# Kernel tuning notes

Measured on AMD Instinct MI355X. Metric: run time of the kernel, lower is better.

Reference implementation:

```python
import jax, jax.numpy as jnp
import numpy as np

B, R, L, K = 64, 196, 512, 768
NEG = jnp.float32(-2**31 + 1)


def setup_inputs() -> dict:
    key = jax.random.key(0)
    ks = jax.random.split(key, 8)
    image_emb = jax.random.normal(ks[0], (B, R, L), dtype=jnp.float32)
    seq_emb = jax.random.normal(ks[1], (B, L, K), dtype=jnp.float32)
    mask = jax.random.randint(ks[2], (B, L), 0, 2, dtype=jnp.int32)
    # Linear(l,1) and Linear(k,1) params, Xavier-ish scale
    image_W = jax.random.normal(ks[3], (L, 1), dtype=jnp.float32) / np.sqrt(L)
    image_b = jnp.zeros((1,), dtype=jnp.float32)
    seq_W = jax.random.normal(ks[4], (K, 1), dtype=jnp.float32) / np.sqrt(K)
    seq_b = jnp.zeros((1,), dtype=jnp.float32)
    # V_weight [L, L], xavier_uniform
    lim = np.sqrt(6.0 / (L + L)).astype(np.float32)
    V_weight = jax.random.uniform(ks[5], (L, L), dtype=jnp.float32, minval=-lim, maxval=lim)
    return {"image_emb": image_emb, "seq_emb": seq_emb, "mask": mask,
            "image_W": image_W, "image_b": image_b,
            "seq_W": seq_W, "seq_b": seq_b, "V_weight": V_weight}


def reference(image_emb, seq_emb, mask, image_W, image_b, seq_W, seq_b, V_weight):
    # p: [B,R,1], q: [B,L,1]
    p = jnp.tanh(image_emb @ image_W + image_b)
    q = jnp.tanh(seq_emb @ seq_W + seq_b)
    qt = jnp.swapaxes(q, 1, 2)              # [B,1,L]
    emb = p @ qt + qt                       # [B,R,L] (rank-1 outer + broadcast add)
    score = emb @ V_weight                  # [B,R,L]
    # dropout_rate=0.0 -> identity
    score = jnp.where(mask[:, None, :] == 0, NEG, score)
    score = jax.nn.softmax(score, axis=-1)  # [B,R,L]
    out = score @ seq_emb                   # [B,R,K]
    out = out / jnp.sqrt(jnp.float32(seq_emb.shape[-1]))
    return out
```

## Files before the change

kernel.cpp:

```cpp
#include <hip/hip_runtime.h>
#include <cstdint>
#include <cstddef>


typedef __attribute__((ext_vector_type(8))) short short8;
typedef __attribute__((ext_vector_type(4))) float f32x4;

__device__ __forceinline__ unsigned short f32_to_bf16(float x) {
    unsigned int u = __float_as_uint(x);
    unsigned int r = (u + 0x7FFFu + ((u >> 16) & 1u)) >> 16;
    return (unsigned short)r;
}
__device__ __forceinline__ float bf16_to_f32(unsigned short h) {
    return __uint_as_float(((unsigned int)h) << 16);
}

__global__ __launch_bounds__(256) void krows_p(const float* __restrict__ x,
                                               const float* __restrict__ w,
                                               const float* __restrict__ bias,
                                               float* __restrict__ outp) {
    int wv = threadIdx.x >> 6, lane = threadIdx.x & 63;
    int row = blockIdx.x * 4 + wv;
    const float4* x4 = (const float4*)(x + (size_t)row * 512);
    const float4* w4 = (const float4*)w;
    float s = 0.f;
#pragma unroll
    for (int i = 0; i < 2; ++i) {
        float4 a = x4[i * 64 + lane];
        float4 c = w4[i * 64 + lane];
        s += a.x * c.x + a.y * c.y + a.z * c.z + a.w * c.w;
    }
#pragma unroll
    for (int o = 32; o; o >>= 1) s += __shfl_xor(s, o, 64);
    if (lane == 0) outp[row] = tanhf(s + bias[0]);
}

__global__ __launch_bounds__(256) void krows_q(const float* __restrict__ x,
                                               const float* __restrict__ w,
                                               const float* __restrict__ bias,
                                               float* __restrict__ outp) {
    int wv = threadIdx.x >> 6, lane = threadIdx.x & 63;
    int row = blockIdx.x * 4 + wv;
    const float4* x4 = (const float4*)(x + (size_t)row * 768);
    const float4* w4 = (const float4*)w;
    float s = 0.f;
#pragma unroll
    for (int i = 0; i < 3; ++i) {
        float4 a = x4[i * 64 + lane];
        float4 c = w4[i * 64 + lane];
        s += a.x * c.x + a.y * c.y + a.z * c.z + a.w * c.w;
    }
#pragma unroll
    for (int o = 32; o; o >>= 1) s += __shfl_xor(s, o, 64);
    if (lane == 0) outp[row] = tanhf(s + bias[0]);
}

__global__ __launch_bounds__(256) void kw(const float* __restrict__ qv,
                                          const float* __restrict__ V,
                                          const int* __restrict__ mask,
                                          float* __restrict__ wm) {
    __shared__ __align__(16) float sq[512];
    __shared__ __align__(16) float sacc[8][32][4];
    int b = blockIdx.x >> 2, jc = blockIdx.x & 3;
    int t = threadIdx.x;
    sq[t] = qv[b * 512 + t];
    sq[t + 256] = qv[b * 512 + t + 256];
    __syncthreads();
    int jt = t & 31, lg = t >> 5;
    const float4* V4 = (const float4*)V;
    int col4 = jc * 32 + jt;
    float ax = 0.f, ay = 0.f, az = 0.f, aw = 0.f;
    int lbase = lg * 64;
#pragma unroll 8
    for (int li = 0; li < 64; ++li) {
        int l = lbase + li;
        float qq = sq[l];
        float4 v = V4[(size_t)l * 128 + col4];
        ax += qq * v.x; ay += qq * v.y; az += qq * v.z; aw += qq * v.w;
    }
    sacc[lg][jt][0] = ax; sacc[lg][jt][1] = ay;
    sacc[lg][jt][2] = az; sacc[lg][jt][3] = aw;
    __syncthreads();
    if (t < 32) {
        float sx = 0.f, sy = 0.f, sz = 0.f, sw = 0.f;
#pragma unroll
        for (int g = 0; g < 8; ++g) {
            sx += sacc[g][t][0]; sy += sacc[g][t][1];
            sz += sacc[g][t][2]; sw += sacc[g][t][3];
        }
        const int* mrow = mask + b * 512 + jc * 128 + t * 4;
        float4 o;
        o.x = mrow[0] ? sx : -1e30f;
        o.y = mrow[1] ? sy : -1e30f;
        o.z = mrow[2] ? sz : -1e30f;
        o.w = mrow[3] ? sw : -1e30f;
        ((float4*)(wm + b * 512 + jc * 128))[t] = o;
    }
}

__global__ __launch_bounds__(256, 2) void kattn(const float* __restrict__ seq,
                                                const float* __restrict__ p,
                                                const float* __restrict__ wm,
                                                float* __restrict__ out) {
    __shared__ __align__(16) unsigned int sseq[2][128 * 32];
    __shared__ __align__(16) float swm[512];
    __shared__ float sinvz[64];
    __shared__ float sred[16];

    int id = blockIdx.x;
    int rt = id & 3;
    int nt = (id >> 2) % 6;
    int b  = id / 24;
    int t  = threadIdx.x;
    int wv = t >> 6, lane = t & 63;
    int mm = lane & 15, q = lane >> 4;
    int nb = nt * 128;

    float v0 = wm[b * 512 + t];
    float v1 = wm[b * 512 + t + 256];
    swm[t] = v0; swm[t + 256] = v1;
    float lmax = fmaxf(v0, v1);
    float fa = (v0 > -1e29f) ? v0 : 1e30f;
    float fb = (v1 > -1e29f) ? v1 : 1e30f;
    float lmin = fminf(fa, fb);
#pragma unroll
    for (int o = 32; o; o >>= 1) {
        lmax = fmaxf(lmax, __shfl_xor(lmax, o, 64));
        lmin = fminf(lmin, __shfl_xor(lmin, o, 64));
    }
    if (lane == 0) { sred[wv] = lmax; sred[8 + wv] = lmin; }
    __syncthreads();
    float wmax = fmaxf(fmaxf(sred[0], sred[1]), fmaxf(sred[2], sred[3]));
    float wmin = fminf(fminf(sred[8], sred[9]), fminf(sred[10], sred[11]));

    int rl = wv * 16 + mm;
    int r  = rt * 64 + rl;
    bool valid = r < 196;
    int pidx = b * 196 + (valid ? r : 195);
    float c = 1.0f + p[pidx];
    float M = (c >= 0.f) ? c * wmax : c * wmin;

    short8 afrag[16];
    float zsum = 0.f;
    const f32x4* swm4 = (const f32x4*)swm;
#pragma unroll
    for (int tk = 0; tk < 16; ++tk) {
        int jb = tk * 32 + q * 8;
        f32x4 w0 = swm4[jb >> 2];
        f32x4 w1 = swm4[(jb >> 2) + 1];
        short8 af;
#pragma unroll
        for (int jj = 0; jj < 8; ++jj) {
            float ww = (jj < 4) ? w0[jj] : w1[jj - 4];
            float e = valid ? __expf(c * ww - M) : 0.f;
            unsigned short h = f32_to_bf16(e);
            zsum += bf16_to_f32(h);
            af[jj] = (short)h;
        }
        afrag[tk] = af;
    }
    zsum += __shfl_xor(zsum, 16, 64);
    zsum += __shfl_xor(zsum, 32, 64);
    if (q == 0) sinvz[rl] = 1.0f / zsum;

    f32x4 acc[8];
#pragma unroll
    for (int s = 0; s < 8; ++s) acc[s] = (f32x4){0.f, 0.f, 0.f, 0.f};

    const float* seqb = seq + (size_t)b * 512 * 768 + nb;
    int tl = t & 31, jp = t >> 5;
    int n0 = tl * 4;
    auto stage = [&](int ch, int buf) {
        unsigned int* sb = sseq[buf];
#pragma unroll
        for (int pass = 0; pass < 4; ++pass) {
            int jl = pass * 16 + jp * 2;
            int jglob = ch * 64 + jl;
            float4 a0 = *(const float4*)(seqb + (size_t)jglob * 768 + n0);
            float4 a1 = *(const float4*)(seqb + (size_t)(jglob + 1) * 768 + n0);
            float a0v[4] = {a0.x, a0.y, a0.z, a0.w};
            float a1v[4] = {a1.x, a1.y, a1.z, a1.w};
            int g = jl >> 3;
            int wo = (jl & 7) >> 1;
#pragma unroll
            for (int i = 0; i < 4; ++i) {
                int n = n0 + i;
                int sw = (n ^ (n >> 3)) & 7;
                unsigned int pk = (unsigned int)f32_to_bf16(a0v[i]) |
                                  ((unsigned int)f32_to_bf16(a1v[i]) << 16);
                sb[n * 32 + ((g ^ sw) << 2) + wo] = pk;
            }
        }
    };

    __syncthreads();
    stage(0, 0);
    __syncthreads();
#pragma unroll
    for (int ch = 0; ch < 8; ++ch) {
        if (ch < 7) stage(ch + 1, (ch + 1) & 1);
        const unsigned int* cb = sseq[ch & 1];
#pragma unroll
        for (int kk = 0; kk < 2; ++kk) {
            short8 bfr[8];
#pragma unroll
            for (int s = 0; s < 8; ++s) {
                int n = s * 16 + mm;
                int g = kk * 4 + q;
                int sw = (n ^ (n >> 3)) & 7;
                bfr[s] = *(const short8*)(cb + n * 32 + ((g ^ sw) << 2));
            }
#pragma unroll
            for (int s = 0; s < 8; ++s)
                acc[s] = __builtin_amdgcn_mfma_f32_16x16x32_bf16(
                    afrag[ch * 2 + kk], bfr[s], acc[s], 0, 0, 0);
        }
        __syncthreads();
    }

    const float invsqrtk = 0.036084391824351615f;
#pragma unroll
    for (int reg = 0; reg < 4; ++reg) {
        int row = q * 4 + reg;
        int rr = rt * 64 + wv * 16 + row;
        if (rr < 196) {
            float scale = sinvz[wv * 16 + row] * invsqrtk;
            float* op = out + (size_t)(b * 196 + rr) * 768 + nb + mm;
#pragma unroll
            for (int s = 0; s < 8; ++s)
                op[s * 16] = acc[s][reg] * scale;
        }
    }
}

extern "C" void kernel_launch(void* const* d_in, const int* in_sizes, int n_in,
                              void* d_out, int out_size, void* d_ws, size_t ws_size,
                              hipStream_t stream) {
    const float* image_emb = (const float*)d_in[0];
    const float* seq_emb   = (const float*)d_in[1];
    const int*   mask      = (const int*)d_in[2];
    const float* image_W   = (const float*)d_in[3];
    const float* image_b   = (const float*)d_in[4];
    const float* seq_W     = (const float*)d_in[5];
    const float* seq_b     = (const float*)d_in[6];
    const float* V         = (const float*)d_in[7];
    float* out = (float*)d_out;

    float* p_ws  = (float*)d_ws;
    float* q_ws  = (float*)((char*)d_ws + (64 << 10));
    float* wm_ws = (float*)((char*)d_ws + (192 << 10));

    krows_p<<<dim3(3136), dim3(256), 0, stream>>>(image_emb, image_W, image_b, p_ws);
    krows_q<<<dim3(8192), dim3(256), 0, stream>>>(seq_emb, seq_W, seq_b, q_ws);
    kw<<<dim3(256), dim3(256), 0, stream>>>(q_ws, V, mask, wm_ws);
    kattn<<<dim3(1536), dim3(256), 0, stream>>>(seq_emb, p_ws, wm_ws, out);
}
```

Measured before the change: 257.6 us.

## Fuse q projection with bf16 transpose of seq_emb and use transposed MFMA attention

Adds a kernel that reads seq_emb once, computes the q projection, and writes a bf16 transposed copy (K-major) to workspace. A new attention kernel stages tiles of that copy into swizzled LDS with double buffering and feeds bf16 MFMA directly, with a block-index remap for locality. The intent is to halve the bytes the attention kernel reads and make its B-operand loads contiguous, in exchange for writing a 50MB intermediate. The old path remains as a fallback when the workspace is too small.

```diff
diff --git a/kernel.cpp b/kernel.cpp
--- a/kernel.cpp
+++ b/kernel.cpp
@@ -53,6 +53,60 @@
 #pragma unroll
     for (int o = 32; o; o >>= 1) s += __shfl_xor(s, o, 64);
     if (lane == 0) outp[row] = tanhf(s + bias[0]);
+}
+
+__global__ __launch_bounds__(256) void ktrans(const float* __restrict__ seq,
+                                              const float* __restrict__ seqW,
+                                              const float* __restrict__ bias,
+                                              unsigned short* __restrict__ seqT,
+                                              float* __restrict__ qv) {
+    __shared__ __align__(16) float sW[768];
+    __shared__ __align__(16) unsigned short sT[128 * 74];
+    int b = blockIdx.x >> 3, jt = blockIdx.x & 7;
+    int j0 = jt * 64;
+    int t = threadIdx.x;
+    sW[t] = seqW[t]; sW[t + 256] = seqW[t + 256]; sW[t + 512] = seqW[t + 512];
+    int rowin = t >> 5, seg = t & 31;
+    const float* base = seq + (size_t)b * 512 * 768 + (size_t)j0 * 768;
+    unsigned short* dstb0 = seqT + (size_t)b * 768 * 512 + j0;
+    int kr8 = t >> 3, jseg = t & 7;
+    float qp[8] = {0.f, 0.f, 0.f, 0.f, 0.f, 0.f, 0.f, 0.f};
+    __syncthreads();
+    for (int ck = 0; ck < 6; ++ck) {
+        if (ck) __syncthreads();
+#pragma unroll
+        for (int p = 0; p < 8; ++p) {
+            int jl = p * 8 + rowin;
+            float4 a = *(const float4*)(base + (size_t)jl * 768 + ck * 128 + seg * 4);
+            float4 w = *(const float4*)(sW + ck * 128 + seg * 4);
+            qp[p] += a.x * w.x + a.y * w.y + a.z * w.z + a.w * w.w;
+            int c0 = seg * 4;
+            sT[(c0 + 0) * 74 + jl] = f32_to_bf16(a.x);
+            sT[(c0 + 1) * 74 + jl] = f32_to_bf16(a.y);
+            sT[(c0 + 2) * 74 + jl] = f32_to_bf16(a.z);
+            sT[(c0 + 3) * 74 + jl] = f32_to_bf16(a.w);
+        }
+        __syncthreads();
+        const unsigned int* sT32 = (const unsigned int*)sT;
+        unsigned short* dstb = dstb0 + (size_t)ck * 128 * 512;
+#pragma unroll
+        for (int wp = 0; wp < 4; ++wp) {
+            int kr = wp * 32 + kr8;
+            uint4 v;
+            v.x = sT32[kr * 37 + jseg * 4 + 0];
+            v.y = sT32[kr * 37 + jseg * 4 + 1];
+            v.z = sT32[kr * 37 + jseg * 4 + 2];
+            v.w = sT32[kr * 37 + jseg * 4 + 3];
+            *(uint4*)(dstb + (size_t)kr * 512 + jseg * 8) = v;
+        }
+    }
+#pragma unroll
+    for (int p = 0; p < 8; ++p) {
+        float s = qp[p];
+#pragma unroll
+        for (int o = 16; o; o >>= 1) s += __shfl_xor(s, o, 64);
+        if ((t & 31) == 0) qv[b * 512 + j0 + p * 8 + rowin] = tanhf(s + bias[0]);
+    }
 }
 
 __global__ __launch_bounds__(256) void kw(const float* __restrict__ qv,
@@ -95,6 +149,127 @@
         o.z = mrow[2] ? sz : -1e30f;
         o.w = mrow[3] ? sw : -1e30f;
         ((float4*)(wm + b * 512 + jc * 128))[t] = o;
+    }
+}
+
+__global__ __launch_bounds__(256, 2) void kattn2(const unsigned short* __restrict__ seqT,
+                                                 const float* __restrict__ p,
+                                                 const float* __restrict__ wm,
+                                                 float* __restrict__ out) {
+    __shared__ __align__(16) unsigned short sB[2][128 * 64];
+    __shared__ __align__(16) float swm[512];
+    __shared__ float sinvz[64];
+    __shared__ float sred[16];
+
+    int raw = blockIdx.x;
+    int g  = ((raw >> 5) << 3) + (raw & 7);
+    int rt = (raw >> 3) & 3;
+    int b  = g / 6, nt = g - b * 6;
+    int t  = threadIdx.x;
+    int wv = t >> 6, lane = t & 63;
+    int mm = lane & 15, q = lane >> 4;
+    int nb = nt * 128;
+
+    float v0 = wm[b * 512 + t];
+    float v1 = wm[b * 512 + t + 256];
+    swm[t] = v0; swm[t + 256] = v1;
+    float lmax = fmaxf(v0, v1);
+    float fa = (v0 > -1e29f) ? v0 : 1e30f;
+    float fb = (v1 > -1e29f) ? v1 : 1e30f;
+    float lmin = fminf(fa, fb);
+#pragma unroll
+    for (int o = 32; o; o >>= 1) {
+        lmax = fmaxf(lmax, __shfl_xor(lmax, o, 64));
+        lmin = fminf(lmin, __shfl_xor(lmin, o, 64));
+    }
+    if (lane == 0) { sred[wv] = lmax; sred[8 + wv] = lmin; }
+    __syncthreads();
+    float wmax = fmaxf(fmaxf(sred[0], sred[1]), fmaxf(sred[2], sred[3]));
+    float wmin = fminf(fminf(sred[8], sred[9]), fminf(sred[10], sred[11]));
+
+    int rl = wv * 16 + mm;
+    int r  = rt * 64 + rl;
+    bool valid = r < 196;
+    int pidx = b * 196 + (valid ? r : 195);
+    float c = 1.0f + p[pidx];
+    float M = (c >= 0.f) ? c * wmax : c * wmin;
+
+    short8 afrag[16];
+    float zsum = 0.f;
+    const f32x4* swm4 = (const f32x4*)swm;
+#pragma unroll
+    for (int tk = 0; tk < 16; ++tk) {
+        int jb = tk * 32 + q * 8;
+        f32x4 w0 = swm4[jb >> 2];
+        f32x4 w1 = swm4[(jb >> 2) + 1];
+        short8 af;
+#pragma unroll
+        for (int jj = 0; jj < 8; ++jj) {
+            float ww = (jj < 4) ? w0[jj] : w1[jj - 4];
+            float e = valid ? __expf(c * ww - M) : 0.f;
+            unsigned short h = f32_to_bf16(e);
+            zsum += bf16_to_f32(h);
+            af[jj] = (short)h;
+        }
+        afrag[tk] = af;
+    }
+    zsum += __shfl_xor(zsum, 16, 64);
+    zsum += __shfl_xor(zsum, 32, 64);
+    if (q == 0) sinvz[rl] = 1.0f / zsum;
+
+    f32x4 acc[8];
+#pragma unroll
+    for (int s = 0; s < 8; ++s) acc[s] = (f32x4){0.f, 0.f, 0.f, 0.f};
+
+    const unsigned short* seqTb = seqT + (size_t)b * 768 * 512 + (size_t)nb * 512;
+    int nrow = t >> 3, jg = t & 7;
+    auto stage = [&](int ch, int buf) {
+        unsigned short* sb = sB[buf];
+#pragma unroll
+        for (int pp = 0; pp < 4; ++pp) {
+            int n = pp * 32 + nrow;
+            short8 v = *(const short8*)(seqTb + (size_t)n * 512 + ch * 64 + jg * 8);
+            int sw = (n ^ (n >> 3)) & 7;
+            *(short8*)(sb + n * 64 + ((jg ^ sw) << 3)) = v;
+        }
+    };
+
+    __syncthreads();
+    stage(0, 0);
+    __syncthreads();
+#pragma unroll
+    for (int ch = 0; ch < 8; ++ch) {
+        if (ch < 7) stage(ch + 1, (ch + 1) & 1);
+        const unsigned short* cb = sB[ch & 1];
+#pragma unroll
+        for (int kk = 0; kk < 2; ++kk) {
+            short8 bfr[8];
+#pragma unroll
+            for (int s = 0; s < 8; ++s) {
+                int n = s * 16 + mm;
+                int sw = (n ^ (n >> 3)) & 7;
+                bfr[s] = *(const short8*)(cb + n * 64 + ((((kk << 2) + q) ^ sw) << 3));
+            }
+#pragma unroll
+            for (int s = 0; s < 8; ++s)
+                acc[s] = __builtin_amdgcn_mfma_f32_16x16x32_bf16(
+                    afrag[(ch << 1) + kk], bfr[s], acc[s], 0, 0, 0);
+        }
+        __syncthreads();
+    }
+
+    const float invsqrtk = 0.036084391824351615f;
+#pragma unroll
+    for (int reg = 0; reg < 4; ++reg) {
+        int row = q * 4 + reg;
+        int rr = rt * 64 + wv * 16 + row;
+        if (rr < 196) {
+            float scale = sinvz[wv * 16 + row] * invsqrtk;
+            float* op = out + (size_t)(b * 196 + rr) * 768 + nb + mm;
+#pragma unroll
+            for (int s = 0; s < 8; ++s)
+                op[s * 16] = acc[s][reg] * scale;
+        }
     }
 }
 
@@ -249,9 +424,17 @@
     float* p_ws  = (float*)d_ws;
     float* q_ws  = (float*)((char*)d_ws + (64 << 10));
     float* wm_ws = (float*)((char*)d_ws + (192 << 10));
-
+    unsigned short* seqT = (unsigned short*)((char*)d_ws + (384 << 10));
+
+    size_t need = (size_t)(384 << 10) + (size_t)64 * 768 * 512 * 2;
     krows_p<<<dim3(3136), dim3(256), 0, stream>>>(image_emb, image_W, image_b, p_ws);
-    krows_q<<<dim3(8192), dim3(256), 0, stream>>>(seq_emb, seq_W, seq_b, q_ws);
-    kw<<<dim3(256), dim3(256), 0, stream>>>(q_ws, V, mask, wm_ws);
-    kattn<<<dim3(1536), dim3(256), 0, stream>>>(seq_emb, p_ws, wm_ws, out);
-}
+    if (ws_size >= need) {
+        ktrans<<<dim3(512), dim3(256), 0, stream>>>(seq_emb, seq_W, seq_b, seqT, q_ws);
+        kw<<<dim3(256), dim3(256), 0, stream>>>(q_ws, V, mask, wm_ws);
+        kattn2<<<dim3(1536), dim3(256), 0, stream>>>(seqT, p_ws, wm_ws, out);
+    } else {
+        krows_q<<<dim3(8192), dim3(256), 0, stream>>>(seq_emb, seq_W, seq_b, q_ws);
+        kw<<<dim3(256), dim3(256), 0, stream>>>(q_ws, V, mask, wm_ws);
+        kattn<<<dim3(1536), dim3(256), 0, stream>>>(seq_emb, p_ws, wm_ws, out);
+    }
+}
```

After: 242.6 us. 1.06x faster.

## Merge row-projection kernels, restage seq tile k-major with packed bf16 stores, remap blocks

Applied to the files above, without the earlier changes.

Combines the p and q projection kernels into one launch so there is one fewer launch and the work shares a grid. In the attention kernel, each thread now loads four consecutive sequence rows and writes packed bf16 pairs as 8-byte LDS stores in a k-major swizzled layout. This cuts shared-store instructions and conversion cost, using the hardware packed bf16 convert when available. Blocks are remapped so that the four row tiles of the same (batch, column tile) run close together, which should improve L2 reuse of seq_emb. The risks are different global-load coalescing patterns and LDS bank behaviour.

```diff
diff --git a/kernel.cpp b/kernel.cpp
--- a/kernel.cpp
+++ b/kernel.cpp
@@ -15,44 +15,60 @@
     return __uint_as_float(((unsigned int)h) << 16);
 }
 
-__global__ __launch_bounds__(256) void krows_p(const float* __restrict__ x,
-                                               const float* __restrict__ w,
-                                               const float* __restrict__ bias,
-                                               float* __restrict__ outp) {
+#if defined(__has_builtin)
+#if __has_builtin(__builtin_amdgcn_cvt_pk_bf16_f32)
+#define HAVE_PK_BF16 1
+#endif
+#endif
+
+__device__ __forceinline__ unsigned int pk_bf16(float a, float b) {
+#ifdef HAVE_PK_BF16
+    typedef __attribute__((ext_vector_type(2))) __bf16 bf16x2;
+    bf16x2 v = __builtin_amdgcn_cvt_pk_bf16_f32(a, b);
+    return __builtin_bit_cast(unsigned int, v);
+#else
+    return (unsigned int)f32_to_bf16(a) | ((unsigned int)f32_to_bf16(b) << 16);
+#endif
+}
+
+__global__ __launch_bounds__(256) void krows(const float* __restrict__ img,
+                                             const float* __restrict__ imgW,
+                                             const float* __restrict__ imgBias,
+                                             const float* __restrict__ seqe,
+                                             const float* __restrict__ seqW,
+                                             const float* __restrict__ seqBias,
+                                             float* __restrict__ pv,
+                                             float* __restrict__ qv) {
     int wv = threadIdx.x >> 6, lane = threadIdx.x & 63;
-    int row = blockIdx.x * 4 + wv;
-    const float4* x4 = (const float4*)(x + (size_t)row * 512);
-    const float4* w4 = (const float4*)w;
-    float s = 0.f;
-#pragma unroll
-    for (int i = 0; i < 2; ++i) {
-        float4 a = x4[i * 64 + lane];
-        float4 c = w4[i * 64 + lane];
-        s += a.x * c.x + a.y * c.y + a.z * c.z + a.w * c.w;
-    }
-#pragma unroll
-    for (int o = 32; o; o >>= 1) s += __shfl_xor(s, o, 64);
-    if (lane == 0) outp[row] = tanhf(s + bias[0]);
-}
-
-__global__ __launch_bounds__(256) void krows_q(const float* __restrict__ x,
-                                               const float* __restrict__ w,
-                                               const float* __restrict__ bias,
-                                               float* __restrict__ outp) {
-    int wv = threadIdx.x >> 6, lane = threadIdx.x & 63;
-    int row = blockIdx.x * 4 + wv;
-    const float4* x4 = (const float4*)(x + (size_t)row * 768);
-    const float4* w4 = (const float4*)w;
-    float s = 0.f;
-#pragma unroll
-    for (int i = 0; i < 3; ++i) {
-        float4 a = x4[i * 64 + lane];
-        float4 c = w4[i * 64 + lane];
-        s += a.x * c.x + a.y * c.y + a.z * c.z + a.w * c.w;
-    }
-#pragma unroll
-    for (int o = 32; o; o >>= 1) s += __shfl_xor(s, o, 64);
-    if (lane == 0) outp[row] = tanhf(s + bias[0]);
+    if (blockIdx.x < 3136) {
+        int row = blockIdx.x * 4 + wv;
+        const float4* x4 = (const float4*)(img + (size_t)row * 512);
+        const float4* w4 = (const float4*)imgW;
+        float s = 0.f;
+#pragma unroll
+        for (int i = 0; i < 2; ++i) {
+            float4 a = x4[i * 64 + lane];
+            float4 c = w4[i * 64 + lane];
+            s += a.x * c.x + a.y * c.y + a.z * c.z + a.w * c.w;
+        }
+#pragma unroll
+        for (int o = 32; o; o >>= 1) s += __shfl_xor(s, o, 64);
+        if (lane == 0) pv[row] = tanhf(s + imgBias[0]);
+    } else {
+        int row = (blockIdx.x - 3136) * 4 + wv;
+        const float4* x4 = (const float4*)(seqe + (size_t)row * 768);
+        const float4* w4 = (const float4*)seqW;
+        float s = 0.f;
+#pragma unroll
+        for (int i = 0; i < 3; ++i) {
+            float4 a = x4[i * 64 + lane];
+            float4 c = w4[i * 64 + lane];
+            s += a.x * c.x + a.y * c.y + a.z * c.z + a.w * c.w;
+        }
+#pragma unroll
+        for (int o = 32; o; o >>= 1) s += __shfl_xor(s, o, 64);
+        if (lane == 0) qv[row] = tanhf(s + seqBias[0]);
+    }
 }
 
 __global__ __launch_bounds__(256) void kw(const float* __restrict__ qv,
@@ -98,19 +114,19 @@
     }
 }
 
-__global__ __launch_bounds__(256, 2) void kattn(const float* __restrict__ seq,
-                                                const float* __restrict__ p,
-                                                const float* __restrict__ wm,
-                                                float* __restrict__ out) {
-    __shared__ __align__(16) unsigned int sseq[2][128 * 32];
+__global__ __launch_bounds__(256, 2) void kattn3(const float* __restrict__ seq,
+                                                 const float* __restrict__ p,
+                                                 const float* __restrict__ wm,
+                                                 float* __restrict__ out) {
+    __shared__ __align__(16) unsigned short sB[2][128 * 64];
     __shared__ __align__(16) float swm[512];
     __shared__ float sinvz[64];
     __shared__ float sred[16];
 
-    int id = blockIdx.x;
-    int rt = id & 3;
-    int nt = (id >> 2) % 6;
-    int b  = id / 24;
+    int raw = blockIdx.x;
+    int g  = ((raw >> 5) << 3) + (raw & 7);
+    int rt = (raw >> 3) & 3;
+    int b  = g / 6, nt = g - b * 6;
     int t  = threadIdx.x;
     int wv = t >> 6, lane = t & 63;
     int mm = lane & 15, q = lane >> 4;
@@ -167,28 +183,31 @@
 #pragma unroll
     for (int s = 0; s < 8; ++s) acc[s] = (f32x4){0.f, 0.f, 0.f, 0.f};
 
+    int quad = t >> 4, kseg = t & 15;
+    int g8 = quad >> 1, sub = quad & 1;
     const float* seqb = seq + (size_t)b * 512 * 768 + nb;
-    int tl = t & 31, jp = t >> 5;
-    int n0 = tl * 4;
     auto stage = [&](int ch, int buf) {
-        unsigned int* sb = sseq[buf];
-#pragma unroll
-        for (int pass = 0; pass < 4; ++pass) {
-            int jl = pass * 16 + jp * 2;
-            int jglob = ch * 64 + jl;
-            float4 a0 = *(const float4*)(seqb + (size_t)jglob * 768 + n0);
-            float4 a1 = *(const float4*)(seqb + (size_t)(jglob + 1) * 768 + n0);
-            float a0v[4] = {a0.x, a0.y, a0.z, a0.w};
-            float a1v[4] = {a1.x, a1.y, a1.z, a1.w};
-            int g = jl >> 3;
-            int wo = (jl & 7) >> 1;
+        unsigned short* sb = sB[buf];
+        const float* src = seqb + (size_t)(ch * 64 + quad * 4) * 768;
+#pragma unroll
+        for (int rp = 0; rp < 2; ++rp) {
+            int k0 = rp * 64 + kseg * 4;
+            float4 r0 = *(const float4*)(src + 0 * 768 + k0);
+            float4 r1 = *(const float4*)(src + 1 * 768 + k0);
+            float4 r2 = *(const float4*)(src + 2 * 768 + k0);
+            float4 r3 = *(const float4*)(src + 3 * 768 + k0);
+            float a0[4] = {r0.x, r0.y, r0.z, r0.w};
+            float a1[4] = {r1.x, r1.y, r1.z, r1.w};
+            float a2[4] = {r2.x, r2.y, r2.z, r2.w};
+            float a3[4] = {r3.x, r3.y, r3.z, r3.w};
 #pragma unroll
             for (int i = 0; i < 4; ++i) {
-                int n = n0 + i;
-                int sw = (n ^ (n >> 3)) & 7;
-                unsigned int pk = (unsigned int)f32_to_bf16(a0v[i]) |
-                                  ((unsigned int)f32_to_bf16(a1v[i]) << 16);
-                sb[n * 32 + ((g ^ sw) << 2) + wo] = pk;
+                int k = k0 + i;
+                int sw = (k ^ (k >> 3)) & 7;
+                uint2 v;
+                v.x = pk_bf16(a0[i], a1[i]);
+                v.y = pk_bf16(a2[i], a3[i]);
+                *(uint2*)(sb + k * 64 + ((g8 ^ sw) << 3) + (sub << 2)) = v;
             }
         }
     };
@@ -199,21 +218,20 @@
 #pragma unroll
     for (int ch = 0; ch < 8; ++ch) {
         if (ch < 7) stage(ch + 1, (ch + 1) & 1);
-        const unsigned int* cb = sseq[ch & 1];
+        const unsigned short* cb = sB[ch & 1];
 #pragma unroll
         for (int kk = 0; kk < 2; ++kk) {
             short8 bfr[8];
 #pragma unroll
             for (int s = 0; s < 8; ++s) {
                 int n = s * 16 + mm;
-                int g = kk * 4 + q;
                 int sw = (n ^ (n >> 3)) & 7;
-                bfr[s] = *(const short8*)(cb + n * 32 + ((g ^ sw) << 2));
+                bfr[s] = *(const short8*)(cb + n * 64 + ((((kk << 2) + q) ^ sw) << 3));
             }
 #pragma unroll
             for (int s = 0; s < 8; ++s)
                 acc[s] = __builtin_amdgcn_mfma_f32_16x16x32_bf16(
-                    afrag[ch * 2 + kk], bfr[s], acc[s], 0, 0, 0);
+                    afrag[(ch << 1) + kk], bfr[s], acc[s], 0, 0, 0);
         }
         __syncthreads();
     }
@@ -250,8 +268,9 @@
     float* q_ws  = (float*)((char*)d_ws + (64 << 10));
     float* wm_ws = (float*)((char*)d_ws + (192 << 10));
 
-    krows_p<<<dim3(3136), dim3(256), 0, stream>>>(image_emb, image_W, image_b, p_ws);
-    krows_q<<<dim3(8192), dim3(256), 0, stream>>>(seq_emb, seq_W, seq_b, q_ws);
+    krows<<<dim3(11328), dim3(256), 0, stream>>>(image_emb, image_W, image_b,
+                                                 seq_emb, seq_W, seq_b,
+                                                 p_ws, q_ws);
     kw<<<dim3(256), dim3(256), 0, stream>>>(q_ws, V, mask, wm_ws);
-    kattn<<<dim3(1536), dim3(256), 0, stream>>>(seq_emb, p_ws, wm_ws, out);
-}
+    kattn3<<<dim3(1536), dim3(256), 0, stream>>>(seq_emb, p_ws, wm_ws, out);
+}
```

Result: faster. 233.6 us (-9.3%).
